# Performance work log

Measured on AMD Instinct MI355X. Metric: run time of the kernel, lower is better.

## Reference

```python
import jax, jax.numpy as jnp
import numpy as np

PRE_NMS = 2000          # _pre_nms_top_n['testing']
POST_NMS = 1000         # _post_nms_top_n['testing']
NMS_THRESH = 0.7
MIN_SIZE = 1.0
BBOX_XFORM_CLIP = float(np.log(1000.0 / 16.0))  # standard dw/dh clamp


def setup_inputs() -> dict:
    key = jax.random.key(0)
    k1, k2, k3, k4, k5 = jax.random.split(key, 5)
    N = 2_000_000
    H, W = 800, 1333
    # realistic anchors: centers uniform over the image, sizes in [16, 256]
    cx = jax.random.uniform(k1, (N,)) * W
    cy = jax.random.uniform(k2, (N,)) * H
    wh = 16.0 + jax.random.uniform(k3, (N, 2)) * 240.0
    anchor = jnp.stack([cx - wh[:, 0] / 2, cy - wh[:, 1] / 2,
                        cx + wh[:, 0] / 2, cy + wh[:, 1] / 2], axis=1)
    objectness = jax.random.normal(k4, (N,))
    pred_bbox_delta = jax.random.normal(k5, (N, 4)) * 0.1
    return {"anchor": anchor, "objectness": objectness,
            "pred_bbox_delta": pred_bbox_delta, "image_h": H, "image_w": W}


def _decode(delta, anchor):
    # BoxCoder.decode with reg_weights = (1,1,1,1)
    w = anchor[:, 2] - anchor[:, 0]
    h = anchor[:, 3] - anchor[:, 1]
    cx = anchor[:, 0] + 0.5 * w
    cy = anchor[:, 1] + 0.5 * h
    dx, dy, dw, dh = delta[:, 0], delta[:, 1], delta[:, 2], delta[:, 3]
    dw = jnp.minimum(dw, BBOX_XFORM_CLIP)
    dh = jnp.minimum(dh, BBOX_XFORM_CLIP)
    pcx = dx * w + cx
    pcy = dy * h + cy
    pw = jnp.exp(dw) * w
    ph = jnp.exp(dh) * h
    return jnp.stack([pcx - 0.5 * pw, pcy - 0.5 * ph,
                      pcx + 0.5 * pw, pcy + 0.5 * ph], axis=1)


def _greedy_nms_keep(boxes, keep_init):
    # boxes: [K,4] already sorted by descending score; keep_init masks invalid boxes
    K = boxes.shape[0]
    areas = (boxes[:, 2] - boxes[:, 0]) * (boxes[:, 3] - boxes[:, 1])
    idx = jnp.arange(K)

    def body(i, keep):
        b = boxes[i]
        xx1 = jnp.maximum(b[0], boxes[:, 0])
        yy1 = jnp.maximum(b[1], boxes[:, 1])
        xx2 = jnp.minimum(b[2], boxes[:, 2])
        yy2 = jnp.minimum(b[3], boxes[:, 3])
        inter = jnp.maximum(xx2 - xx1, 0.0) * jnp.maximum(yy2 - yy1, 0.0)
        iou = inter / (areas[i] + areas - inter + 1e-9)
        suppress = (iou > NMS_THRESH) & (idx > i) & keep[i]
        return keep & ~suppress

    return jax.lax.fori_loop(0, K, body, keep_init)


def reference(anchor, objectness, pred_bbox_delta, image_h, image_w):
    # 1) top-k pre-NMS selection over all N anchors (memory-bound)
    score, top_idx = jax.lax.top_k(objectness, PRE_NMS)
    a = anchor[top_idx]
    d = pred_bbox_delta[top_idx]
    # 2) box decode
    boxes = _decode(d, a)
    # 3) clip to image (process_box)
    x1 = jnp.clip(boxes[:, 0], 0.0, float(image_w))
    y1 = jnp.clip(boxes[:, 1], 0.0, float(image_h))
    x2 = jnp.clip(boxes[:, 2], 0.0, float(image_w))
    y2 = jnp.clip(boxes[:, 3], 0.0, float(image_h))
    boxes = jnp.stack([x1, y1, x2, y2], axis=1)
    # 4) min-size filter -> mask (fixed shapes under jit)
    valid = ((x2 - x1) >= MIN_SIZE) & ((y2 - y1) >= MIN_SIZE)
    # 5) greedy NMS (boxes are already score-sorted; invalid never kept/suppressing)
    keep = _greedy_nms_keep(boxes, valid)
    # 6) take first POST_NMS kept boxes; pad the rest with zeros
    neg_inf = jnp.float32(-jnp.inf)
    final_score = jnp.where(keep, score, neg_inf)
    fs, fi = jax.lax.top_k(final_score, POST_NMS)
    mask = jnp.isfinite(fs)[:, None].astype(boxes.dtype)
    proposal = boxes[fi] * mask  # [POST_NMS, 4], zero-padded
    return proposal
```

## Files before the change

kernel.cpp:

```cpp
#include <hip/hip_runtime.h>
#include <hip/hip_bf16.h>


typedef unsigned int uint;
typedef unsigned long long ull;

#define PRE_NMS   2000
#define POST_NMS  1000
#define SORT_N    4096
#define NBINS     2048
#define NMS_TH    0.7f
#define MIN_SIZE  1.0f
#define BBOX_CLIP 4.135166556742356f

#define HIST_OFF    0
#define META_OFF    8192
#define VALID_OFF   8448
#define CAND_OFF    8704
#define TOPIDX_OFF  41472
#define BOXES_OFF   49472
#define MASK_OFF    81472
#define REM_OFF     593472
#define ZERO_WORDS  2176

__device__ __forceinline__ uint map_f32(float f) {
    uint u = __float_as_uint(f);
    return u ^ ((u & 0x80000000u) ? 0xFFFFFFFFu : 0x80000000u);
}

__global__ __launch_bounds__(256) void init_kernel(uint* __restrict__ wsHead,
                                                   float4* __restrict__ out) {
    int t = blockIdx.x * 256 + threadIdx.x;
    if (t < ZERO_WORDS) wsHead[t] = 0u;
    if (t < POST_NMS) out[t] = make_float4(0.f, 0.f, 0.f, 0.f);
}

__global__ __launch_bounds__(256) void hist_kernel(const float* __restrict__ obj,
                                                   int n, uint* __restrict__ hist) {
    __shared__ uint h[NBINS];
    for (int b = threadIdx.x; b < NBINS; b += 256) h[b] = 0;
    __syncthreads();
    int n4 = n >> 2;
    const float4* obj4 = reinterpret_cast<const float4*>(obj);
    int stride = gridDim.x * blockDim.x;
    for (int i = blockIdx.x * blockDim.x + threadIdx.x; i < n4; i += stride) {
        float4 v = obj4[i];
        atomicAdd(&h[map_f32(v.x) >> 21], 1u);
        atomicAdd(&h[map_f32(v.y) >> 21], 1u);
        atomicAdd(&h[map_f32(v.z) >> 21], 1u);
        atomicAdd(&h[map_f32(v.w) >> 21], 1u);
    }
    int base = n4 << 2;
    for (int i = base + blockIdx.x * blockDim.x + threadIdx.x; i < n; i += stride)
        atomicAdd(&h[map_f32(obj[i]) >> 21], 1u);
    __syncthreads();
    for (int b = threadIdx.x; b < NBINS; b += 256)
        if (h[b]) atomicAdd(&hist[b], h[b]);
}

__global__ __launch_bounds__(256) void thresh_kernel(const uint* __restrict__ hist,
                                                     uint* __restrict__ meta) {
    __shared__ uint s_sum[256];
    __shared__ uint s_suf[256];
    int t = threadIdx.x;
    uint local[8];
    uint sum = 0;
#pragma unroll 8
    for (int b = 0; b < 8; b++) { local[b] = hist[t * 8 + b]; sum += local[b]; }
    s_sum[t] = sum;
    __syncthreads();
    if (t == 0) {
        uint acc = 0;
        for (int c = 255; c >= 0; c--) { s_suf[c] = acc; acc += s_sum[c]; }
    }
    __syncthreads();
    uint c = s_suf[t];
#pragma unroll 8
    for (int b = 7; b >= 0; b--) {
        uint nc = c + local[b];
        if (c < (uint)PRE_NMS && nc >= (uint)PRE_NMS) meta[0] = (uint)(t * 8 + b);
        c = nc;
    }
}

__global__ __launch_bounds__(256) void collect_kernel(const float* __restrict__ obj,
                                                      int n, uint* __restrict__ meta,
                                                      ull* __restrict__ cand) {
    uint T = meta[0];
    int n4 = n >> 2;
    const float4* obj4 = reinterpret_cast<const float4*>(obj);
    int stride = gridDim.x * blockDim.x;
    for (int i = blockIdx.x * blockDim.x + threadIdx.x; i < n4; i += stride) {
        float4 v = obj4[i];
        uint u0 = map_f32(v.x), u1 = map_f32(v.y), u2 = map_f32(v.z), u3 = map_f32(v.w);
        if ((u0 >> 21) >= T) {
            uint pos = atomicAdd(&meta[1], 1u);
            if (pos < (uint)SORT_N) cand[pos] = ((ull)u0 << 32) | (ull)(~(uint)(i * 4 + 0));
        }
        if ((u1 >> 21) >= T) {
            uint pos = atomicAdd(&meta[1], 1u);
            if (pos < (uint)SORT_N) cand[pos] = ((ull)u1 << 32) | (ull)(~(uint)(i * 4 + 1));
        }
        if ((u2 >> 21) >= T) {
            uint pos = atomicAdd(&meta[1], 1u);
            if (pos < (uint)SORT_N) cand[pos] = ((ull)u2 << 32) | (ull)(~(uint)(i * 4 + 2));
        }
        if ((u3 >> 21) >= T) {
            uint pos = atomicAdd(&meta[1], 1u);
            if (pos < (uint)SORT_N) cand[pos] = ((ull)u3 << 32) | (ull)(~(uint)(i * 4 + 3));
        }
    }
    int base = n4 << 2;
    for (int i = base + blockIdx.x * blockDim.x + threadIdx.x; i < n; i += stride) {
        uint u = map_f32(obj[i]);
        if ((u >> 21) >= T) {
            uint pos = atomicAdd(&meta[1], 1u);
            if (pos < (uint)SORT_N) cand[pos] = ((ull)u << 32) | (ull)(~(uint)i);
        }
    }
}

__global__ __launch_bounds__(1024) void sort_kernel(const ull* __restrict__ cand,
                                                    const uint* __restrict__ meta,
                                                    int* __restrict__ topIdx) {
    __shared__ ull keys[SORT_N];
    uint n = meta[1]; if (n > (uint)SORT_N) n = SORT_N;
    for (int t = threadIdx.x; t < SORT_N; t += 1024)
        keys[t] = (t < (int)n) ? cand[t] : 0ULL;
    __syncthreads();
    for (int k = 2; k <= SORT_N; k <<= 1) {
        for (int j = k >> 1; j > 0; j >>= 1) {
            for (int t = threadIdx.x; t < SORT_N; t += 1024) {
                int ixj = t ^ j;
                if (ixj > t) {
                    ull A = keys[t], B = keys[ixj];
                    bool desc = ((t & k) == 0);
                    if (desc ? (A < B) : (A > B)) { keys[t] = B; keys[ixj] = A; }
                }
            }
            __syncthreads();
        }
    }
    for (int t = threadIdx.x; t < PRE_NMS; t += 1024)
        topIdx[t] = (int)(~(uint)keys[t]);
}

__global__ __launch_bounds__(256) void decode_kernel(const float* __restrict__ anchor,
                                                     const float* __restrict__ delta,
                                                     const int* __restrict__ topIdx,
                                                     const int* __restrict__ imh,
                                                     const int* __restrict__ imw,
                                                     float4* __restrict__ boxes,
                                                     ull* __restrict__ validWords) {
    int i = blockIdx.x * blockDim.x + threadIdx.x;
    if (i >= PRE_NMS) return;
    int idx = topIdx[i];
    const float4 a = reinterpret_cast<const float4*>(anchor)[idx];
    const float4 d = reinterpret_cast<const float4*>(delta)[idx];
    float W = (float)imw[0], H = (float)imh[0];
    float w  = a.z - a.x;
    float h  = a.w - a.y;
    float cx = a.x + 0.5f * w;
    float cy = a.y + 0.5f * h;
    float dw = fminf(d.z, BBOX_CLIP);
    float dh = fminf(d.w, BBOX_CLIP);
    float pcx = d.x * w + cx;
    float pcy = d.y * h + cy;
    float pw  = expf(dw) * w;
    float ph  = expf(dh) * h;
    float x1 = fminf(fmaxf(pcx - 0.5f * pw, 0.0f), W);
    float y1 = fminf(fmaxf(pcy - 0.5f * ph, 0.0f), H);
    float x2 = fminf(fmaxf(pcx + 0.5f * pw, 0.0f), W);
    float y2 = fminf(fmaxf(pcy + 0.5f * ph, 0.0f), H);
    boxes[i] = make_float4(x1, y1, x2, y2);
    bool valid = (x2 - x1 >= MIN_SIZE) && (y2 - y1 >= MIN_SIZE);
    if (valid) atomicOr(&validWords[i >> 6], 1ULL << (i & 63));
}

__global__ __launch_bounds__(256) void mask_kernel(const float4* __restrict__ boxes,
                                                   ull* __restrict__ mask) {
    __shared__ float4 b[PRE_NMS];
    for (int t = threadIdx.x; t < PRE_NMS; t += 256) b[t] = boxes[t];
    __syncthreads();
    int tid = blockIdx.x * 256 + threadIdx.x;
    int i = tid >> 5, w = tid & 31;
    if (i >= PRE_NMS) return;
    float4 bi = b[i];
    float areai = (bi.z - bi.x) * (bi.w - bi.y);
    ull m = 0;
    int j0 = w * 64;
    for (int jj = 0; jj < 64; jj++) {
        int j = j0 + jj;
        if (j < PRE_NMS && j > i) {
            float4 bj = b[j];
            float xx1 = fmaxf(bi.x, bj.x), yy1 = fmaxf(bi.y, bj.y);
            float xx2 = fminf(bi.z, bj.z), yy2 = fminf(bi.w, bj.w);
            float inter = fmaxf(xx2 - xx1, 0.0f) * fmaxf(yy2 - yy1, 0.0f);
            float areaj = (bj.z - bj.x) * (bj.w - bj.y);
            float iou = inter / (areai + areaj - inter + 1e-9f);
            if (iou > NMS_TH) m |= (1ULL << jj);
        }
    }
    mask[i * 32 + w] = m;
}

__device__ __forceinline__ void nms_stage_block(const char* mb, ull* dst,
                                                int w, int lane) {
    const size_t base = (size_t)w * 16384;
#pragma unroll
    for (int k = 0; k < 16; ++k) {
        size_t off = base + (size_t)k * 1024;
        const char* src = (off + 1024 <= (size_t)PRE_NMS * 256) ? (mb + off) : mb;
        __builtin_amdgcn_global_load_lds(
            (const __attribute__((address_space(1))) uint*)(src + lane * 16),
            (__attribute__((address_space(3))) uint*)((char*)dst + k * 1024),
            16, 0, 0);
    }
}

__global__ __launch_bounds__(64) void nms_kernel(const ull* __restrict__ mask,
                                                 const ull* __restrict__ validWords,
                                                 ull* __restrict__ remOut) {
    __shared__ ull buf[2][2048];
    const int lane = threadIdx.x;
    ull rem = (lane < 32) ? ~validWords[lane] : ~0ULL;
    const char* mb = (const char*)mask;

    nms_stage_block(mb, &buf[0][0], 0, lane);

    for (int w = 0; w < 32; ++w) {
        const int b = w & 1;
        if (w + 1 < 32) {
            nms_stage_block(mb, &buf[b ^ 1][0], w + 1, lane);
            asm volatile("s_waitcnt vmcnt(16)" ::: "memory");
        } else {
            asm volatile("s_waitcnt vmcnt(0)" ::: "memory");
        }
        __builtin_amdgcn_sched_barrier(0);

        ull remw = __shfl(rem, w);
        const int nrow = PRE_NMS - w * 64 < 64 ? PRE_NMS - w * 64 : 64;
        const int lw = lane & 31;
#pragma unroll
        for (int i = 0; i < 64; ++i) {
            ull d = buf[b][i * 32 + w];
            ull o = buf[b][i * 32 + lw];
            bool act = (i < nrow) && !((remw >> i) & 1ULL);
            ull sel = act ? ~0ULL : 0ULL;
            remw |= d & sel;
            rem  |= o & sel;
        }
    }
    if (lane < 32) remOut[lane] = rem;
}

__global__ __launch_bounds__(256) void output_kernel(const float4* __restrict__ boxes,
                                                     const ull* __restrict__ rem,
                                                     float4* __restrict__ out) {
    __shared__ uint pre[33];
    __shared__ ull kept_s[32];
    int t = threadIdx.x;
    if (t < 32) kept_s[t] = ~rem[t];
    __syncthreads();
    if (t == 0) {
        uint acc = 0;
        for (int w = 0; w < 32; w++) { pre[w] = acc; acc += (uint)__popcll(kept_s[w]); }
        pre[32] = acc;
    }
    __syncthreads();
    for (int i = t; i < PRE_NMS; i += 256) {
        ull kw = kept_s[i >> 6];
        if ((kw >> (i & 63)) & 1ULL) {
            uint rank = pre[i >> 6] +
                        (uint)__popcll(kw & ((1ULL << (i & 63)) - 1ULL));
            if (rank < (uint)POST_NMS) out[rank] = boxes[i];
        }
    }
}

extern "C" void kernel_launch(void* const* d_in, const int* in_sizes, int n_in,
                              void* d_out, int out_size, void* d_ws, size_t ws_size,
                              hipStream_t stream) {
    const float* anchor = (const float*)d_in[0];
    const float* obj    = (const float*)d_in[1];
    const float* delta  = (const float*)d_in[2];
    const int*   imh    = (const int*)d_in[3];
    const int*   imw    = (const int*)d_in[4];
    int n = in_sizes[1];

    char* ws = (char*)d_ws;
    uint* hist       = (uint*)(ws + HIST_OFF);
    uint* meta       = (uint*)(ws + META_OFF);
    ull*  validWords = (ull*)(ws + VALID_OFF);
    ull*  cand       = (ull*)(ws + CAND_OFF);
    int*  topIdx     = (int*)(ws + TOPIDX_OFF);
    float4* boxes    = (float4*)(ws + BOXES_OFF);
    ull*  mask       = (ull*)(ws + MASK_OFF);
    ull*  rem        = (ull*)(ws + REM_OFF);

    init_kernel<<<(ZERO_WORDS + 255) / 256, 256, 0, stream>>>(
        (uint*)ws, (float4*)d_out);
    hist_kernel<<<512, 256, 0, stream>>>(obj, n, hist);
    thresh_kernel<<<1, 256, 0, stream>>>(hist, meta);
    collect_kernel<<<512, 256, 0, stream>>>(obj, n, meta, cand);
    sort_kernel<<<1, 1024, 0, stream>>>(cand, meta, topIdx);
    decode_kernel<<<(PRE_NMS + 255) / 256, 256, 0, stream>>>(
        anchor, delta, topIdx, imh, imw, boxes, validWords);
    mask_kernel<<<(PRE_NMS * 32 + 255) / 256, 256, 0, stream>>>(boxes, mask);
    nms_kernel<<<1, 64, 0, stream>>>(mask, validWords, rem);
    output_kernel<<<1, 256, 0, stream>>>(boxes, rem, (float4*)d_out);
}
```

Before: 317.3 us.

## Store NMS mask column-major with XOR-swizzled LDS staging and vectorized reads

The IoU mask is now written column-major (one 2048-row column per 64-box chunk), and mask_kernel assigns threads so adjacent threads write adjacent rows. The NMS kernel stages each chunk with an XOR swizzle into LDS and reads rows as 16-byte vectors, double-buffering register chunks, so the serial suppression loop does fewer, bank-conflict-free LDS loads. The bit test is now branchless (bit-1 mask). The mask buffer grows to 2048 padded rows and the indexing becomes more intricate.

```diff
diff --git a/kernel.cpp b/kernel.cpp
--- a/kernel.cpp
+++ b/kernel.cpp
@@ -13,6 +13,8 @@
 #define MIN_SIZE  1.0f
 #define BBOX_CLIP 4.135166556742356f
 
+#define CM_ROWS   2048
+
 #define HIST_OFF    0
 #define META_OFF    8192
 #define VALID_OFF   8448
@@ -20,7 +22,7 @@
 #define TOPIDX_OFF  41472
 #define BOXES_OFF   49472
 #define MASK_OFF    81472
-#define REM_OFF     593472
+#define REM_OFF     605760
 #define ZERO_WORDS  2176
 
 __device__ __forceinline__ uint map_f32(float f) {
@@ -178,53 +180,60 @@
 }
 
 __global__ __launch_bounds__(256) void mask_kernel(const float4* __restrict__ boxes,
-                                                   ull* __restrict__ mask) {
+                                                   ull* __restrict__ maskCM) {
     __shared__ float4 b[PRE_NMS];
     for (int t = threadIdx.x; t < PRE_NMS; t += 256) b[t] = boxes[t];
     __syncthreads();
     int tid = blockIdx.x * 256 + threadIdx.x;
-    int i = tid >> 5, w = tid & 31;
-    if (i >= PRE_NMS) return;
-    float4 bi = b[i];
-    float areai = (bi.z - bi.x) * (bi.w - bi.y);
+    int c = tid >> 11;
+    int r = tid & (CM_ROWS - 1);
     ull m = 0;
-    int j0 = w * 64;
-    for (int jj = 0; jj < 64; jj++) {
-        int j = j0 + jj;
-        if (j < PRE_NMS && j > i) {
-            float4 bj = b[j];
-            float xx1 = fmaxf(bi.x, bj.x), yy1 = fmaxf(bi.y, bj.y);
-            float xx2 = fminf(bi.z, bj.z), yy2 = fminf(bi.w, bj.w);
-            float inter = fmaxf(xx2 - xx1, 0.0f) * fmaxf(yy2 - yy1, 0.0f);
-            float areaj = (bj.z - bj.x) * (bj.w - bj.y);
-            float iou = inter / (areai + areaj - inter + 1e-9f);
-            if (iou > NMS_TH) m |= (1ULL << jj);
-        }
-    }
-    mask[i * 32 + w] = m;
-}
-
-__device__ __forceinline__ void nms_stage_block(const char* mb, ull* dst,
+    if (r < PRE_NMS) {
+        float4 bi = b[r];
+        float areai = (bi.z - bi.x) * (bi.w - bi.y);
+        int j0 = c * 64;
+#pragma unroll
+        for (int jj = 0; jj < 64; jj++) {
+            int j = j0 + jj;
+            if (j < PRE_NMS && j > r) {
+                float4 bj = b[j];
+                float xx1 = fmaxf(bi.x, bj.x), yy1 = fmaxf(bi.y, bj.y);
+                float xx2 = fminf(bi.z, bj.z), yy2 = fminf(bi.w, bj.w);
+                float inter = fmaxf(xx2 - xx1, 0.0f) * fmaxf(yy2 - yy1, 0.0f);
+                float areaj = (bj.z - bj.x) * (bj.w - bj.y);
+                float iou = inter / (areai + areaj - inter + 1e-9f);
+                if (iou > NMS_TH) m |= (1ULL << jj);
+            }
+        }
+    }
+    maskCM[tid] = m;
+}
+
+__device__ __forceinline__ void nms_stage_block(const char* mb, void* dst,
                                                 int w, int lane) {
-    const size_t base = (size_t)w * 16384;
+    const int c0 = lane >> 5;
+    const int u  = lane & 31;
 #pragma unroll
     for (int k = 0; k < 16; ++k) {
-        size_t off = base + (size_t)k * 1024;
-        const char* src = (off + 1024 <= (size_t)PRE_NMS * 256) ? (mb + off) : mb;
+        const int c = 2 * k + c0;
+        const int q = u ^ (c & 15);
+        const char* src = mb + (size_t)c * (CM_ROWS * 8)
+                             + (size_t)w * 512 + (size_t)(q * 16);
         __builtin_amdgcn_global_load_lds(
-            (const __attribute__((address_space(1))) uint*)(src + lane * 16),
+            (const __attribute__((address_space(1))) uint*)src,
             (__attribute__((address_space(3))) uint*)((char*)dst + k * 1024),
             16, 0, 0);
     }
 }
 
-__global__ __launch_bounds__(64) void nms_kernel(const ull* __restrict__ mask,
+__global__ __launch_bounds__(64) void nms_kernel(const ull* __restrict__ maskCM,
                                                  const ull* __restrict__ validWords,
                                                  ull* __restrict__ remOut) {
-    __shared__ ull buf[2][2048];
+    __shared__ __align__(16) ull buf[2][2048];
     const int lane = threadIdx.x;
+    const int lw = lane & 31;
     ull rem = (lane < 32) ? ~validWords[lane] : ~0ULL;
-    const char* mb = (const char*)mask;
+    const char* mb = (const char*)maskCM;
 
     nms_stage_block(mb, &buf[0][0], 0, lane);
 
@@ -239,16 +248,40 @@
         __builtin_amdgcn_sched_barrier(0);
 
         ull remw = __shfl(rem, w);
-        const int nrow = PRE_NMS - w * 64 < 64 ? PRE_NMS - w * 64 : 64;
-        const int lw = lane & 31;
-#pragma unroll
-        for (int i = 0; i < 64; ++i) {
-            ull d = buf[b][i * 32 + w];
-            ull o = buf[b][i * 32 + lw];
-            bool act = (i < nrow) && !((remw >> i) & 1ULL);
-            ull sel = act ? ~0ULL : 0ULL;
-            remw |= d & sel;
-            rem  |= o & sel;
+        const char* ldsb = (const char*)&buf[b][0];
+        const char* dcol = ldsb + 512 * w;
+        const char* ocol = ldsb + 512 * lw;
+        const int sw = (w & 15) << 4;
+        const int so = (lw & 15) << 4;
+
+        ulonglong2 dA[8], oA[8], dB[8], oB[8];
+#pragma unroll
+        for (int q = 0; q < 8; ++q) {
+            dA[q] = *(const ulonglong2*)(dcol + ((q << 4) ^ sw));
+            oA[q] = *(const ulonglong2*)(ocol + ((q << 4) ^ so));
+        }
+#pragma unroll
+        for (int ch = 0; ch < 4; ++ch) {
+            if (ch < 3) {
+#pragma unroll
+                for (int q = 0; q < 8; ++q) {
+                    const int qg = (ch + 1) * 8 + q;
+                    dB[q] = *(const ulonglong2*)(dcol + ((qg << 4) ^ sw));
+                    oB[q] = *(const ulonglong2*)(ocol + ((qg << 4) ^ so));
+                }
+            }
+#pragma unroll
+            for (int t = 0; t < 16; ++t) {
+                const int i = ch * 16 + t;
+                ull d = (t & 1) ? dA[t >> 1].y : dA[t >> 1].x;
+                ull o = (t & 1) ? oA[t >> 1].y : oA[t >> 1].x;
+                ull bit = (remw >> i) & 1ULL;
+                ull sel = bit - 1ULL;
+                remw |= d & sel;
+                rem  |= o & sel;
+            }
+#pragma unroll
+            for (int q = 0; q < 8; ++q) { dA[q] = dB[q]; oA[q] = oB[q]; }
         }
     }
     if (lane < 32) remOut[lane] = rem;
@@ -295,7 +328,7 @@
     ull*  cand       = (ull*)(ws + CAND_OFF);
     int*  topIdx     = (int*)(ws + TOPIDX_OFF);
     float4* boxes    = (float4*)(ws + BOXES_OFF);
-    ull*  mask       = (ull*)(ws + MASK_OFF);
+    ull*  maskCM     = (ull*)(ws + MASK_OFF);
     ull*  rem        = (ull*)(ws + REM_OFF);
 
     init_kernel<<<(ZERO_WORDS + 255) / 256, 256, 0, stream>>>(
@@ -306,7 +339,7 @@
     sort_kernel<<<1, 1024, 0, stream>>>(cand, meta, topIdx);
     decode_kernel<<<(PRE_NMS + 255) / 256, 256, 0, stream>>>(
         anchor, delta, topIdx, imh, imw, boxes, validWords);
-    mask_kernel<<<(PRE_NMS * 32 + 255) / 256, 256, 0, stream>>>(boxes, mask);
-    nms_kernel<<<1, 64, 0, stream>>>(mask, validWords, rem);
+    mask_kernel<<<(32 * CM_ROWS) / 256, 256, 0, stream>>>(boxes, maskCM);
+    nms_kernel<<<1, 64, 0, stream>>>(maskCM, validWords, rem);
     output_kernel<<<1, 256, 0, stream>>>(boxes, rem, (float4*)d_out);
 }
```

New measurement: 290.0 us. 1.09x faster.

## Restructure serial NMS scan to use readlane broadcasts and split-half row processing

Applied to the files above, without the earlier changes.

The serial NMS kernel now has each half of the wavefront handle alternating mask rows. Suppression bits for the current diagonal word are gathered with readlane instead of separate LDS reads, and the two halves' removed-masks are merged at the end with one shuffle. The mask kernel pads its grid to 2048 rows and writes zeros for out-of-range rows, so staging no longer needs bounds checks. The workspace offset moves to fit the larger mask. The goal is a shorter dependent critical path in the single-wave NMS loop, paid for with more readlane instructions and a slightly larger mask buffer.

```diff
diff --git a/kernel.cpp b/kernel.cpp
--- a/kernel.cpp
+++ b/kernel.cpp
@@ -20,7 +20,7 @@
 #define TOPIDX_OFF  41472
 #define BOXES_OFF   49472
 #define MASK_OFF    81472
-#define REM_OFF     593472
+#define REM_OFF     605760
 #define ZERO_WORDS  2176
 
 __device__ __forceinline__ uint map_f32(float f) {
@@ -178,80 +178,107 @@
 }
 
 __global__ __launch_bounds__(256) void mask_kernel(const float4* __restrict__ boxes,
-                                                   ull* __restrict__ mask) {
+                                                   ull* __restrict__ gmask) {
     __shared__ float4 b[PRE_NMS];
     for (int t = threadIdx.x; t < PRE_NMS; t += 256) b[t] = boxes[t];
     __syncthreads();
     int tid = blockIdx.x * 256 + threadIdx.x;
-    int i = tid >> 5, w = tid & 31;
-    if (i >= PRE_NMS) return;
-    float4 bi = b[i];
-    float areai = (bi.z - bi.x) * (bi.w - bi.y);
+    int r = tid >> 5;
+    int c = tid & 31;
     ull m = 0;
-    int j0 = w * 64;
-    for (int jj = 0; jj < 64; jj++) {
-        int j = j0 + jj;
-        if (j < PRE_NMS && j > i) {
-            float4 bj = b[j];
-            float xx1 = fmaxf(bi.x, bj.x), yy1 = fmaxf(bi.y, bj.y);
-            float xx2 = fminf(bi.z, bj.z), yy2 = fminf(bi.w, bj.w);
-            float inter = fmaxf(xx2 - xx1, 0.0f) * fmaxf(yy2 - yy1, 0.0f);
-            float areaj = (bj.z - bj.x) * (bj.w - bj.y);
-            float iou = inter / (areai + areaj - inter + 1e-9f);
-            if (iou > NMS_TH) m |= (1ULL << jj);
-        }
-    }
-    mask[i * 32 + w] = m;
-}
-
-__device__ __forceinline__ void nms_stage_block(const char* mb, ull* dst,
-                                                int w, int lane) {
-    const size_t base = (size_t)w * 16384;
+    if (r < PRE_NMS) {
+        float4 bi = b[r];
+        float areai = (bi.z - bi.x) * (bi.w - bi.y);
+        int j0 = c * 64;
+#pragma unroll
+        for (int jj = 0; jj < 64; jj++) {
+            int j = j0 + jj;
+            if (j < PRE_NMS && j > r) {
+                float4 bj = b[j];
+                float xx1 = fmaxf(bi.x, bj.x), yy1 = fmaxf(bi.y, bj.y);
+                float xx2 = fminf(bi.z, bj.z), yy2 = fminf(bi.w, bj.w);
+                float inter = fmaxf(xx2 - xx1, 0.0f) * fmaxf(yy2 - yy1, 0.0f);
+                float areaj = (bj.z - bj.x) * (bj.w - bj.y);
+                float iou = inter / (areai + areaj - inter + 1e-9f);
+                if (iou > NMS_TH) m |= (1ULL << jj);
+            }
+        }
+    }
+    gmask[tid] = m;
+}
+
+__device__ __forceinline__ void nms_stage_tile(const char* gm, void* dst,
+                                               int w, int lane) {
+    const char* src = gm + (size_t)w * 16384 + (size_t)(lane * 16);
 #pragma unroll
     for (int k = 0; k < 16; ++k) {
-        size_t off = base + (size_t)k * 1024;
-        const char* src = (off + 1024 <= (size_t)PRE_NMS * 256) ? (mb + off) : mb;
         __builtin_amdgcn_global_load_lds(
-            (const __attribute__((address_space(1))) uint*)(src + lane * 16),
+            (const __attribute__((address_space(1))) uint*)(src + k * 1024),
             (__attribute__((address_space(3))) uint*)((char*)dst + k * 1024),
             16, 0, 0);
     }
 }
 
-__global__ __launch_bounds__(64) void nms_kernel(const ull* __restrict__ mask,
+__global__ __launch_bounds__(64) void nms_kernel(const ull* __restrict__ gmask,
                                                  const ull* __restrict__ validWords,
                                                  ull* __restrict__ remOut) {
-    __shared__ ull buf[2][2048];
+    __shared__ __align__(16) ull buf[2][2048];
     const int lane = threadIdx.x;
-    ull rem = (lane < 32) ? ~validWords[lane] : ~0ULL;
-    const char* mb = (const char*)mask;
-
-    nms_stage_block(mb, &buf[0][0], 0, lane);
+    const int lw = lane & 31;
+    const bool hiHalf = lane >= 32;
+    ull rem = hiHalf ? 0ULL : ~validWords[lw];
+    const char* gm = (const char*)gmask;
+
+    nms_stage_tile(gm, &buf[0][0], 0, lane);
 
     for (int w = 0; w < 32; ++w) {
         const int b = w & 1;
         if (w + 1 < 32) {
-            nms_stage_block(mb, &buf[b ^ 1][0], w + 1, lane);
+            nms_stage_tile(gm, &buf[b ^ 1][0], w + 1, lane);
             asm volatile("s_waitcnt vmcnt(16)" ::: "memory");
         } else {
             asm volatile("s_waitcnt vmcnt(0)" ::: "memory");
         }
         __builtin_amdgcn_sched_barrier(0);
 
-        ull remw = __shfl(rem, w);
-        const int nrow = PRE_NMS - w * 64 < 64 ? PRE_NMS - w * 64 : 64;
-        const int lw = lane & 31;
-#pragma unroll
-        for (int i = 0; i < 64; ++i) {
-            ull d = buf[b][i * 32 + w];
-            ull o = buf[b][i * 32 + lw];
-            bool act = (i < nrow) && !((remw >> i) & 1ULL);
-            ull sel = act ? ~0ULL : 0ULL;
-            remw |= d & sel;
-            rem  |= o & sel;
-        }
-    }
-    if (lane < 32) remOut[lane] = rem;
+        const int w32 = w + 32;
+        uint r0 = (uint)__builtin_amdgcn_readlane((int)(uint)rem, w);
+        uint r1 = (uint)__builtin_amdgcn_readlane((int)(uint)(rem >> 32), w);
+        uint r2 = (uint)__builtin_amdgcn_readlane((int)(uint)rem, w32);
+        uint r3 = (uint)__builtin_amdgcn_readlane((int)(uint)(rem >> 32), w32);
+        ull rw = (((ull)(r1 | r3)) << 32) | (ull)(r0 | r2);
+
+        const char* base = (const char*)&buf[b][0] + (hiHalf ? 256 : 0) + lw * 8;
+
+#pragma unroll
+        for (int ch = 0; ch < 4; ++ch) {
+            ull o[8];
+#pragma unroll
+            for (int p = 0; p < 8; ++p)
+                o[p] = *(const ull*)(base + (ch * 16 + 2 * p) * 256);
+#pragma unroll
+            for (int p = 0; p < 8; ++p) {
+                const int i0 = ch * 16 + 2 * p, i1 = i0 + 1;
+                uint dlo0 = (uint)__builtin_amdgcn_readlane((int)(uint)o[p], w);
+                uint dhi0 = (uint)__builtin_amdgcn_readlane((int)(uint)(o[p] >> 32), w);
+                uint dlo1 = (uint)__builtin_amdgcn_readlane((int)(uint)o[p], w32);
+                uint dhi1 = (uint)__builtin_amdgcn_readlane((int)(uint)(o[p] >> 32), w32);
+                ull d0 = (((ull)dhi0) << 32) | dlo0;
+                ull d1 = (((ull)dhi1) << 32) | dlo1;
+                bool a0 = ((rw >> i0) & 1ULL) == 0ULL;
+                rw |= a0 ? d0 : 0ULL;
+                bool a1 = ((rw >> i1) & 1ULL) == 0ULL;
+                rw |= a1 ? d1 : 0ULL;
+                uint m0 = a0 ? ~0u : 0u;
+                uint m1 = a1 ? ~0u : 0u;
+                uint ms = hiHalf ? m1 : m0;
+                rem |= o[p] & ((((ull)ms) << 32) | (ull)ms);
+            }
+        }
+    }
+    ull other = __shfl(rem, lane + 32, 64);
+    rem |= other;
+    if (lane < 32) remOut[lw] = rem;
 }
 
 __global__ __launch_bounds__(256) void output_kernel(const float4* __restrict__ boxes,
@@ -295,7 +322,7 @@
     ull*  cand       = (ull*)(ws + CAND_OFF);
     int*  topIdx     = (int*)(ws + TOPIDX_OFF);
     float4* boxes    = (float4*)(ws + BOXES_OFF);
-    ull*  mask       = (ull*)(ws + MASK_OFF);
+    ull*  gmask      = (ull*)(ws + MASK_OFF);
     ull*  rem        = (ull*)(ws + REM_OFF);
 
     init_kernel<<<(ZERO_WORDS + 255) / 256, 256, 0, stream>>>(
@@ -306,7 +333,7 @@
     sort_kernel<<<1, 1024, 0, stream>>>(cand, meta, topIdx);
     decode_kernel<<<(PRE_NMS + 255) / 256, 256, 0, stream>>>(
         anchor, delta, topIdx, imh, imw, boxes, validWords);
-    mask_kernel<<<(PRE_NMS * 32 + 255) / 256, 256, 0, stream>>>(boxes, mask);
-    nms_kernel<<<1, 64, 0, stream>>>(mask, validWords, rem);
+    mask_kernel<<<(32 * 2048) / 256, 256, 0, stream>>>(boxes, gmask);
+    nms_kernel<<<1, 64, 0, stream>>>(gmask, validWords, rem);
     output_kernel<<<1, 256, 0, stream>>>(boxes, rem, (float4*)d_out);
 }
```

Measured after the change: 310.2 us. 2.2% less time.
